# Kernel tuning notes

Measured on AMD Instinct MI355X. Metric: run time of the kernel, lower is better.

The kernel has to match this reference:

```python
import jax, jax.numpy as jnp
import numpy as np

N_NODES = 50000
N_EDGES = 800000
IN_DIM = 128
HID = 128
NUM_CLASSES = 2


def setup_inputs() -> dict:
    key = jax.random.key(0)
    ks = jax.random.split(key, 16)
    inp = {
        "adj_row": jax.random.randint(ks[0], (N_EDGES,), 0, N_NODES),
        "adj_col": jax.random.randint(ks[1], (N_EDGES,), 0, N_NODES),
        "adj_vals": jax.random.uniform(ks[2], (N_EDGES,), dtype=jnp.float32),
        "input_feature": jax.random.normal(ks[3], (N_NODES, IN_DIM), dtype=jnp.float32),
        "graph_indicator": jax.random.randint(ks[4], (N_NODES,), 0, 64),
        # GCN layer params (kaiming-uniform-ish init; zeros bias like the torch module)
        "W1": jax.random.uniform(ks[5], (IN_DIM, HID), jnp.float32, -1, 1) * np.sqrt(6.0 / IN_DIM),
        "b1": jnp.zeros((HID,), jnp.float32),
        "W2": jax.random.uniform(ks[6], (HID, HID), jnp.float32, -1, 1) * np.sqrt(6.0 / HID),
        "b2": jnp.zeros((HID,), jnp.float32),
        "W3": jax.random.uniform(ks[7], (HID, HID), jnp.float32, -1, 1) * np.sqrt(6.0 / HID),
        "b3": jnp.zeros((HID,), jnp.float32),
        # fc params (torch.nn.Linear default init range)
        "fcW1": jax.random.uniform(ks[8], (3 * HID, HID), jnp.float32, -1, 1) / np.sqrt(3 * HID),
        "fcb1": jax.random.uniform(ks[9], (HID,), jnp.float32, -1, 1) / np.sqrt(3 * HID),
        "fcW2": jax.random.uniform(ks[10], (HID, HID // 2), jnp.float32, -1, 1) / np.sqrt(HID),
        "fcb2": jax.random.uniform(ks[11], (HID // 2,), jnp.float32, -1, 1) / np.sqrt(HID),
        "fcW3": jax.random.uniform(ks[12], (HID // 2, NUM_CLASSES), jnp.float32, -1, 1) / np.sqrt(HID // 2),
        "fcb3": jax.random.uniform(ks[13], (NUM_CLASSES,), jnp.float32, -1, 1) / np.sqrt(HID // 2),
    }
    return inp


def _gcn_layer(row, col, vals, x, W, b, n_nodes):
    # support = X @ W  -> dense GEMM
    support = x @ W
    # sparse.mm(A, support): out[i] = sum_{e: row[e]=i} vals[e] * support[col[e]]
    msgs = support[col] * vals[:, None]  # [E, D] gather + scale
    agg = jax.ops.segment_sum(msgs, row, num_segments=n_nodes)
    return agg + b


def reference(adj_row, adj_col, adj_vals, input_feature, graph_indicator,
              W1, b1, W2, b2, W3, b3, fcW1, fcb1, fcW2, fcb2, fcW3, fcb3):
    n = input_feature.shape[0]
    g1 = jax.nn.relu(_gcn_layer(adj_row, adj_col, adj_vals, input_feature, W1, b1, n))
    g2 = jax.nn.relu(_gcn_layer(adj_row, adj_col, adj_vals, g1, W2, b2, n))
    g3 = jax.nn.relu(_gcn_layer(adj_row, adj_col, adj_vals, g2, W3, b3, n))
    feat = jnp.concatenate([g1, g2, g3], axis=1)  # [N, 3*HID]
    h = jax.nn.relu(feat @ fcW1 + fcb1)
    h = jax.nn.relu(h @ fcW2 + fcb2)
    logits = h @ fcW3 + fcb3
    return logits
```

## Files before the change

### kernel.cpp

```cpp
#include <hip/hip_runtime.h>
#include <hip/hip_bf16.h>

#define N_NODES 50000
#define N_EDGES 800000
#define NBK 391
#define BCAP 2560
#define PADSLACK 896

static inline int cdiv(int a, int b) { return (a + b - 1) / b; }

typedef __attribute__((ext_vector_type(8))) short short8;
typedef __attribute__((ext_vector_type(4))) float f32x4;

__device__ __forceinline__ float b2f(unsigned short u) {
    union { unsigned int i; float f; } c;
    c.i = ((unsigned int)u) << 16;
    return c.f;
}
__device__ __forceinline__ unsigned short f2bb(float f) {
    __hip_bfloat16 h = __float2bfloat16(f);
    return *(unsigned short*)&h;
}

__device__ __forceinline__ void pack_one(const float* __restrict__ W,
                                         __hip_bfloat16* __restrict__ out,
                                         int K, int N, int t) {
    int lane = t & 63;
    int kc = (t >> 6) % (K / 32);
    int nt = (t >> 6) / (K / 32);
    int kbase = kc * 32 + (lane >> 4) * 8;
    int col = nt * 16 + (lane & 15);
    __hip_bfloat16* dst = out + (size_t)t * 8;
#pragma unroll
    for (int j = 0; j < 8; ++j)
        dst[j] = __float2bfloat16(W[(size_t)(kbase + j) * N + col]);
}

__global__ __launch_bounds__(256)
void stage1_kernel(const int* __restrict__ row, const int* __restrict__ col,
                   const float* __restrict__ vals, int* __restrict__ bcursor,
                   int2* __restrict__ tmp, int E,
                   const float* __restrict__ x, __hip_bfloat16* __restrict__ support,
                   int M,
                   const float* __restrict__ W1, const float* __restrict__ W2,
                   const float* __restrict__ W3, const float* __restrict__ fcW1,
                   const float* __restrict__ fcW2,
                   __hip_bfloat16* __restrict__ pW2, __hip_bfloat16* __restrict__ pW3,
                   __hip_bfloat16* __restrict__ pfcW1, __hip_bfloat16* __restrict__ pfcW2) {
    __shared__ unsigned short As[64][136];
    __shared__ int hist[NBK];
    __shared__ int base[NBK];
    const int b = blockIdx.x;
    const int tid = threadIdx.x;

    if (b < 196) {
        const int CH = 4096;
        int e0 = b * CH;
        for (int i = tid; i < NBK; i += 256) hist[i] = 0;
        __syncthreads();
        for (int i = tid; i < CH; i += 256) {
            int e = e0 + i;
            if (e < E) atomicAdd(&hist[row[e] >> 7], 1);
        }
        __syncthreads();
        for (int i = tid; i < NBK; i += 256) {
            int c = hist[i];
            base[i] = (c > 0) ? (i * BCAP + atomicAdd(&bcursor[i], c)) : 0;
            hist[i] = 0;
        }
        __syncthreads();
        for (int i = tid; i < CH; i += 256) {
            int e = e0 + i;
            if (e < E) {
                int r = row[e];
                int bk = r >> 7;
                int rk = atomicAdd(&hist[bk], 1);
                tmp[base[bk] + rk] = make_int2(((r & 127) << 16) | col[e],
                                               __float_as_int(vals[e]));
            }
        }
        return;
    }

    if (b < 978) {
        const int wave = tid >> 6;
        const int lane = tid & 63;
        const int ln15 = lane & 15;
        const int quad = lane >> 4;
        const int m0 = (b - 196) * 64;

        short8 bfr[4][2];
#pragma unroll
        for (int kc = 0; kc < 4; ++kc)
#pragma unroll
            for (int h = 0; h < 2; ++h)
#pragma unroll
                for (int j = 0; j < 8; ++j)
                    bfr[kc][h][j] = (short)f2bb(
                        W1[(size_t)(kc * 32 + quad * 8 + j) * 128 + (wave * 2 + h) * 16 + ln15]);

#pragma unroll
        for (int i = 0; i < 4; ++i) {
            int idx = tid + i * 256;
            int r = idx >> 4;
            int c8 = (idx & 15) * 8;
            uint4 pk = {0, 0, 0, 0};
            if (m0 + r < M) {
                const float* src = &x[(size_t)(m0 + r) * 128 + c8];
                float4 a = *(const float4*)src;
                float4 bq = *(const float4*)(src + 4);
                pk.x = f2bb(a.x) | ((unsigned int)f2bb(a.y) << 16);
                pk.y = f2bb(a.z) | ((unsigned int)f2bb(a.w) << 16);
                pk.z = f2bb(bq.x) | ((unsigned int)f2bb(bq.y) << 16);
                pk.w = f2bb(bq.z) | ((unsigned int)f2bb(bq.w) << 16);
            }
            *(uint4*)&As[r][c8] = pk;
        }
        __syncthreads();

        f32x4 acc[4][2];
#pragma unroll
        for (int s = 0; s < 4; ++s)
#pragma unroll
            for (int h = 0; h < 2; ++h) acc[s][h] = (f32x4){0.f, 0.f, 0.f, 0.f};
#pragma unroll
        for (int kc = 0; kc < 4; ++kc) {
            short8 af[4];
#pragma unroll
            for (int s = 0; s < 4; ++s)
                af[s] = *(const short8*)&As[s * 16 + ln15][kc * 32 + quad * 8];
#pragma unroll
            for (int s = 0; s < 4; ++s)
#pragma unroll
                for (int h = 0; h < 2; ++h)
                    acc[s][h] = __builtin_amdgcn_mfma_f32_16x16x32_bf16(
                        af[s], bfr[kc][h], acc[s][h], 0, 0, 0);
        }
#pragma unroll
        for (int s = 0; s < 4; ++s)
#pragma unroll
            for (int h = 0; h < 2; ++h) {
                int cl = (wave * 2 + h) * 16 + ln15;
#pragma unroll
                for (int r = 0; r < 4; ++r) {
                    int rw = m0 + s * 16 + quad * 4 + r;
                    if (rw < M)
                        support[(size_t)rw * 128 + cl] = __float2bfloat16(acc[s][h][r]);
                }
            }
        return;
    }

    int pb = b - 978;
    if (pb < 8)       pack_one(W2,  pW2,  128, 128, pb * 256 + tid);
    else if (pb < 16) pack_one(W3,  pW3,  128, 128, (pb - 8) * 256 + tid);
    else if (pb < 40) pack_one(fcW1, pfcW1, 384, 128, (pb - 16) * 256 + tid);
    else              pack_one(fcW2, pfcW2, 128, 64, (pb - 40) * 256 + tid);
}

__global__ __launch_bounds__(256)
void binB_kernel(const int2* __restrict__ tmp, const int* __restrict__ bcursor,
                 int2* __restrict__ rowrange, int2* __restrict__ epack, int N) {
    int b = blockIdx.x;
    int r0 = b << 7;
    int nr = N - r0; if (nr > 128) nr = 128;
    __shared__ int cnt[128];
    __shared__ int cur[128];
    __shared__ int rpos[128];
    __shared__ int red[256];
    int t = threadIdx.x;
    int partial = 0;
    for (int i = t; i < b; i += 256) partial += bcursor[i];
    red[t] = partial;
    if (t < 128) cnt[t] = 0;
    __syncthreads();
    for (int off = 128; off > 0; off >>= 1) {
        if (t < off) red[t] += red[t + off];
        __syncthreads();
    }
    int slab = b * BCAP;
    int send = slab + bcursor[b];
    for (int i = slab + t; i < send; i += 256)
        atomicAdd(&cnt[tmp[i].x >> 16], 1);
    __syncthreads();
    int rcnt = (t < 128) ? cnt[t] : 0;
    int pc = (rcnt + 7) & ~7;
    if (t < 128) cur[t] = pc;
    __syncthreads();
    for (int off = 1; off < 128; off <<= 1) {
        int u = (t >= off && t < 128) ? cur[t - off] : 0;
        __syncthreads();
        if (t < 128) cur[t] += u;
        __syncthreads();
    }
    int obase = red[0] + b * PADSLACK;
    if (t < 128) {
        int pos = obase + cur[t] - pc;
        rpos[t] = pos;
        cur[t] = pos;
        if (t < nr) rowrange[r0 + t] = make_int2(pos, pos + pc);
    }
    __syncthreads();
    for (int i = slab + t; i < send; i += 256) {
        int2 v = tmp[i];
        int rl = v.x >> 16;
        int c = v.x & 0xffff;
        int pos = atomicAdd(&cur[rl], 1);
        epack[pos] = make_int2(c, v.y);
    }
    if (t < 128) {
        int rc = rcnt;
        int pos = rpos[t];
#pragma unroll 1
        for (int i = pos + rc; i < pos + pc; ++i)
            epack[i] = make_int2(0, 0);
    }
}

__device__ __forceinline__ void accum8(float* acc, long long e, uint4 u) {
    float f = __int_as_float((int)(e >> 32));
    acc[0] += f * b2f((unsigned short)(u.x & 0xffff));
    acc[1] += f * b2f((unsigned short)(u.x >> 16));
    acc[2] += f * b2f((unsigned short)(u.y & 0xffff));
    acc[3] += f * b2f((unsigned short)(u.y >> 16));
    acc[4] += f * b2f((unsigned short)(u.z & 0xffff));
    acc[5] += f * b2f((unsigned short)(u.z >> 16));
    acc[6] += f * b2f((unsigned short)(u.w & 0xffff));
    acc[7] += f * b2f((unsigned short)(u.w >> 16));
}

__device__ __forceinline__ void agg_node(const long long* __restrict__ ep,
                                         const __hip_bfloat16* __restrict__ support,
                                         int p, int end, int g, int j, float* acc) {
#pragma unroll
    for (int k = 0; k < 8; ++k) acc[k] = 0.f;
    long long e0 = 0, e1 = 0;
    uint4 u0 = {0, 0, 0, 0}, u1 = {0, 0, 0, 0};
    bool have = false;
    if (p < end) {
        e0 = ep[p + g];
        e1 = ep[p + 4 + g];
        u0 = *(const uint4*)&support[(size_t)(unsigned int)(e0 & 0xffffffffu) * 128 + j * 8];
        u1 = *(const uint4*)&support[(size_t)(unsigned int)(e1 & 0xffffffffu) * 128 + j * 8];
        p += 8;
        have = true;
    }
    while (p < end) {
        long long f0 = ep[p + g];
        long long f1 = ep[p + 4 + g];
        uint4 w0 = *(const uint4*)&support[(size_t)(unsigned int)(f0 & 0xffffffffu) * 128 + j * 8];
        uint4 w1 = *(const uint4*)&support[(size_t)(unsigned int)(f1 & 0xffffffffu) * 128 + j * 8];
        accum8(acc, e0, u0);
        accum8(acc, e1, u1);
        e0 = f0; u0 = w0; e1 = f1; u1 = w1;
        p += 8;
    }
    if (have) {
        accum8(acc, e0, u0);
        accum8(acc, e1, u1);
    }
#pragma unroll
    for (int k = 0; k < 8; ++k) {
        acc[k] += __shfl_xor(acc[k], 16);
        acc[k] += __shfl_xor(acc[k], 32);
    }
}

__device__ __forceinline__ uint4 pack_row8(const float* acc, float4 b0, float4 b1) {
    unsigned int q0 = (unsigned int)f2bb(fmaxf(acc[0] + b0.x, 0.f))
                    | ((unsigned int)f2bb(fmaxf(acc[1] + b0.y, 0.f)) << 16);
    unsigned int q1 = (unsigned int)f2bb(fmaxf(acc[2] + b0.z, 0.f))
                    | ((unsigned int)f2bb(fmaxf(acc[3] + b0.w, 0.f)) << 16);
    unsigned int q2 = (unsigned int)f2bb(fmaxf(acc[4] + b1.x, 0.f))
                    | ((unsigned int)f2bb(fmaxf(acc[5] + b1.y, 0.f)) << 16);
    unsigned int q3 = (unsigned int)f2bb(fmaxf(acc[6] + b1.z, 0.f))
                    | ((unsigned int)f2bb(fmaxf(acc[7] + b1.w, 0.f)) << 16);
    return (uint4){q0, q1, q2, q3};
}

__global__ __launch_bounds__(256, 8)
void spmm_gemm_kernel(const int2* __restrict__ rowrange,
                      const int2* __restrict__ epack,
                      const __hip_bfloat16* __restrict__ support,
                      const float* __restrict__ bias,
                      __hip_bfloat16* __restrict__ gout,
                      const __hip_bfloat16* __restrict__ pW,
                      __hip_bfloat16* __restrict__ Cout,
                      int N) {
    __shared__ unsigned short As[16][136];
    const int tid = threadIdx.x;
    const int wv = tid >> 6;
    const int l = tid & 63;
    const int g = l >> 4;
    const int j = l & 15;
    const int m0 = blockIdx.x * 16;
    const long long* ep = (const long long*)epack;
    float4 b0 = *(const float4*)&bias[j * 8];
    float4 b1 = *(const float4*)&bias[j * 8 + 4];

    for (int i = 0; i < 4; ++i) {
        int node = m0 + wv * 4 + i;
        if (node < N) {
            int2 rr = rowrange[node];
            float acc[8];
            agg_node(ep, support, rr.x, rr.y, g, j, acc);
            if (g == 0) {
                uint4 st = pack_row8(acc, b0, b1);
                *(uint4*)&As[wv * 4 + i][j * 8] = st;
                *(uint4*)&gout[(size_t)node * 384 + j * 8] = st;
            }
        } else if (g == 0) {
            *(uint4*)&As[wv * 4 + i][j * 8] = (uint4){0, 0, 0, 0};
        }
    }
    __syncthreads();

    const int ln15 = l & 15;
    const int quad = l >> 4;
    f32x4 acc2[2];
    acc2[0] = (f32x4){0.f, 0.f, 0.f, 0.f};
    acc2[1] = (f32x4){0.f, 0.f, 0.f, 0.f};
#pragma unroll
    for (int kc = 0; kc < 4; ++kc) {
        short8 af = *(const short8*)&As[ln15][kc * 32 + quad * 8];
#pragma unroll
        for (int h = 0; h < 2; ++h) {
            int nt = wv * 2 + h;
            short8 bf = *(const short8*)&pW[((size_t)(nt * 4 + kc) * 64 + l) * 8];
            acc2[h] = __builtin_amdgcn_mfma_f32_16x16x32_bf16(af, bf, acc2[h], 0, 0, 0);
        }
    }
#pragma unroll
    for (int h = 0; h < 2; ++h) {
        int cl = (wv * 2 + h) * 16 + ln15;
#pragma unroll
        for (int r = 0; r < 4; ++r) {
            int rw = m0 + quad * 4 + r;
            if (rw < N)
                Cout[(size_t)rw * 128 + cl] = __float2bfloat16(acc2[h][r]);
        }
    }
}

__global__ __launch_bounds__(256, 8)
void spmm_fc_kernel(const int2* __restrict__ rowrange,
                    const int2* __restrict__ epack,
                    const __hip_bfloat16* __restrict__ support,
                    const float* __restrict__ bias,
                    const __hip_bfloat16* __restrict__ featb,
                    const __hip_bfloat16* __restrict__ pfcW1,
                    const float* __restrict__ fcb1,
                    const __hip_bfloat16* __restrict__ pfcW2,
                    const float* __restrict__ fcb2,
                    const float* __restrict__ fcW3, const float* __restrict__ fcb3,
                    float* __restrict__ out, int N) {
    __shared__ unsigned short As[16][136];
    __shared__ float w3s[128];
    __shared__ float b3s[2];
    const int tid = threadIdx.x;
    const int wv = tid >> 6;
    const int l = tid & 63;
    const int g = l >> 4;
    const int j = l & 15;
    const int m0 = blockIdx.x * 16;
    const long long* ep = (const long long*)epack;
    if (tid < 128) w3s[tid] = fcW3[tid];
    if (tid < 2) b3s[tid] = fcb3[tid];
    float4 b0 = *(const float4*)&bias[j * 8];
    float4 b1 = *(const float4*)&bias[j * 8 + 4];

    for (int i = 0; i < 4; ++i) {
        int node = m0 + wv * 4 + i;
        if (node < N) {
            int2 rr = rowrange[node];
            float acc[8];
            agg_node(ep, support, rr.x, rr.y, g, j, acc);
            if (g == 0)
                *(uint4*)&As[wv * 4 + i][j * 8] = pack_row8(acc, b0, b1);
        } else if (g == 0) {
            *(uint4*)&As[wv * 4 + i][j * 8] = (uint4){0, 0, 0, 0};
        }
    }
    __syncthreads();

    const int ln15 = l & 15;
    const int quad = l >> 4;
    f32x4 acc[2];
    acc[0] = (f32x4){0.f, 0.f, 0.f, 0.f};
    acc[1] = (f32x4){0.f, 0.f, 0.f, 0.f};
#pragma unroll
    for (int step = 0; step < 3; ++step) {
        const int kb = (step == 0) ? 2 : (step - 1);
        if (step != 0) {
            __syncthreads();
            int r = tid >> 4;
            int c8 = (tid & 15) * 8;
            *(uint4*)&As[r][c8] =
                *(const uint4*)&featb[(size_t)(m0 + r) * 384 + kb * 128 + c8];
            __syncthreads();
        }
#pragma unroll
        for (int kc = 0; kc < 4; ++kc) {
            short8 af = *(const short8*)&As[ln15][kc * 32 + quad * 8];
            int kcg = kb * 4 + kc;
#pragma unroll
            for (int h = 0; h < 2; ++h) {
                int nt = wv * 2 + h;
                short8 bf = *(const short8*)&pfcW1[((size_t)(nt * 12 + kcg) * 64 + l) * 8];
                acc[h] = __builtin_amdgcn_mfma_f32_16x16x32_bf16(af, bf, acc[h], 0, 0, 0);
            }
        }
    }
    __syncthreads();
#pragma unroll
    for (int h = 0; h < 2; ++h) {
        int col = (wv * 2 + h) * 16 + ln15;
        float bv = fcb1[col];
#pragma unroll
        for (int r = 0; r < 4; ++r)
            As[quad * 4 + r][col] = f2bb(fmaxf(acc[h][r] + bv, 0.f));
    }
    __syncthreads();

    f32x4 acc2 = (f32x4){0.f, 0.f, 0.f, 0.f};
#pragma unroll
    for (int kc = 0; kc < 4; ++kc) {
        short8 af = *(const short8*)&As[ln15][kc * 32 + quad * 8];
        short8 bfw = *(const short8*)&pfcW2[((size_t)(wv * 4 + kc) * 64 + l) * 8];
        acc2 = __builtin_amdgcn_mfma_f32_16x16x32_bf16(af, bfw, acc2, 0, 0, 0);
    }
    __syncthreads();
    {
        int col2 = wv * 16 + ln15;
        float bv = fcb2[col2];
#pragma unroll
        for (int r = 0; r < 4; ++r)
            As[quad * 4 + r][col2] = f2bb(fmaxf(acc2[r] + bv, 0.f));
    }
    __syncthreads();

    if (tid < 32) {
        int row = tid >> 1, cls = tid & 1;
        int grow = m0 + row;
        if (grow < N) {
            float a = b3s[cls];
#pragma unroll
            for (int k = 0; k < 64; ++k)
                a += b2f(As[row][k]) * w3s[k * 2 + cls];
            out[(size_t)grow * 2 + cls] = a;
        }
    }
}

extern "C" void kernel_launch(void* const* d_in, const int* in_sizes, int n_in,
                              void* d_out, int out_size, void* d_ws, size_t ws_size,
                              hipStream_t stream) {
    const int*   adj_row  = (const int*)d_in[0];
    const int*   adj_col  = (const int*)d_in[1];
    const float* adj_vals = (const float*)d_in[2];
    const float* x        = (const float*)d_in[3];
    const float* W1   = (const float*)d_in[5];
    const float* b1   = (const float*)d_in[6];
    const float* W2   = (const float*)d_in[7];
    const float* b2   = (const float*)d_in[8];
    const float* W3   = (const float*)d_in[9];
    const float* b3   = (const float*)d_in[10];
    const float* fcW1 = (const float*)d_in[11];
    const float* fcb1 = (const float*)d_in[12];
    const float* fcW2 = (const float*)d_in[13];
    const float* fcb2 = (const float*)d_in[14];
    const float* fcW3 = (const float*)d_in[15];
    const float* fcb3 = (const float*)d_in[16];
    float* out = (float*)d_out;

    const int N = N_NODES, E = N_EDGES;
    const int Mpad = 50048;
    const int EPAD = E + NBK * PADSLACK + 64;

    char* p = (char*)d_ws;
    auto alloc = [&](size_t bytes) {
        char* q = p;
        p += (bytes + 255) & ~(size_t)255;
        return q;
    };
    __hip_bfloat16* featb    = (__hip_bfloat16*)alloc((size_t)Mpad * 384 * 2);
    __hip_bfloat16* supportb = (__hip_bfloat16*)alloc((size_t)Mpad * 128 * 2);
    __hip_bfloat16* supportc = (__hip_bfloat16*)alloc((size_t)Mpad * 128 * 2);
    __hip_bfloat16* pW2   = (__hip_bfloat16*)alloc(16384 * 2);
    __hip_bfloat16* pW3   = (__hip_bfloat16*)alloc(16384 * 2);
    __hip_bfloat16* pfcW1 = (__hip_bfloat16*)alloc(49152 * 2);
    __hip_bfloat16* pfcW2 = (__hip_bfloat16*)alloc(8192 * 2);
    int2*  rowrange  = (int2*)alloc((size_t)(N + 1) * 8);
    int*   bcursor   = (int*)alloc((size_t)NBK * 4);
    int2*  epack     = (int2*)alloc((size_t)EPAD * 8);
    int2*  tmp       = (int2*)alloc((size_t)NBK * BCAP * 8);

    hipMemsetAsync(bcursor, 0, (size_t)NBK * 4, stream);
    stage1_kernel<<<1022, 256, 0, stream>>>(adj_row, adj_col, adj_vals, bcursor, tmp, E,
                                            x, supportb, N,
                                            W1, W2, W3, fcW1, fcW2,
                                            pW2, pW3, pfcW1, pfcW2);
    binB_kernel<<<NBK, 256, 0, stream>>>(tmp, bcursor, rowrange, epack, N);

    const int fgrid = cdiv(N, 16);

    spmm_gemm_kernel<<<fgrid, 256, 0, stream>>>(rowrange, epack, supportb, b1,
                                                featb + 0, pW2, supportc, N);
    spmm_gemm_kernel<<<fgrid, 256, 0, stream>>>(rowrange, epack, supportc, b2,
                                                featb + 128, pW3, supportb, N);
    spmm_fc_kernel<<<fgrid, 256, 0, stream>>>(rowrange, epack, supportb, b3,
                                              featb, pfcW1, fcb1, pfcW2, fcb2,
                                              fcW3, fcb3, out, N);
}
```

Before: 252.3 us.

## Bin edges by 16-row blocks and fuse per-row sort into first SpMM

Edge binning now uses 16-row buckets matching the SpMM tile, and the separate binB kernel is removed. The first SpMM+GEMM kernel counts and scatters its own bucket into per-row padded ranges before aggregating, dropping one kernel launch and the global prefix scan. The trade-off is a larger shared histogram in stage1 (3125 bins), fixed per-bucket capacities of 448 edges that could overflow on skewed graphs, and a serial 16-row scan inside each block.

```diff
diff --git a/kernel.cpp b/kernel.cpp
--- a/kernel.cpp
+++ b/kernel.cpp
@@ -3,9 +3,9 @@
 
 #define N_NODES 50000
 #define N_EDGES 800000
-#define NBK 391
-#define BCAP 2560
-#define PADSLACK 896
+#define NB16 3125
+#define BCAP16 448
+#define REG16 560
 
 static inline int cdiv(int a, int b) { return (a + b - 1) / b; }
 
@@ -47,36 +47,37 @@
                    const float* __restrict__ fcW2,
                    __hip_bfloat16* __restrict__ pW2, __hip_bfloat16* __restrict__ pW3,
                    __hip_bfloat16* __restrict__ pfcW1, __hip_bfloat16* __restrict__ pfcW2) {
-    __shared__ unsigned short As[64][136];
-    __shared__ int hist[NBK];
-    __shared__ int base[NBK];
+    __shared__ union {
+        unsigned short As[64][136];
+        struct { int hist[NB16]; int base[NB16]; } bin;
+    } sh;
     const int b = blockIdx.x;
     const int tid = threadIdx.x;
 
     if (b < 196) {
         const int CH = 4096;
         int e0 = b * CH;
-        for (int i = tid; i < NBK; i += 256) hist[i] = 0;
+        for (int i = tid; i < NB16; i += 256) sh.bin.hist[i] = 0;
         __syncthreads();
         for (int i = tid; i < CH; i += 256) {
             int e = e0 + i;
-            if (e < E) atomicAdd(&hist[row[e] >> 7], 1);
+            if (e < E) atomicAdd(&sh.bin.hist[row[e] >> 4], 1);
         }
         __syncthreads();
-        for (int i = tid; i < NBK; i += 256) {
-            int c = hist[i];
-            base[i] = (c > 0) ? (i * BCAP + atomicAdd(&bcursor[i], c)) : 0;
-            hist[i] = 0;
+        for (int i = tid; i < NB16; i += 256) {
+            int c = sh.bin.hist[i];
+            sh.bin.base[i] = (c > 0) ? (i * BCAP16 + atomicAdd(&bcursor[i], c)) : 0;
+            sh.bin.hist[i] = 0;
         }
         __syncthreads();
         for (int i = tid; i < CH; i += 256) {
             int e = e0 + i;
             if (e < E) {
                 int r = row[e];
-                int bk = r >> 7;
-                int rk = atomicAdd(&hist[bk], 1);
-                tmp[base[bk] + rk] = make_int2(((r & 127) << 16) | col[e],
-                                               __float_as_int(vals[e]));
+                int bk = r >> 4;
+                int rk = atomicAdd(&sh.bin.hist[bk], 1);
+                tmp[sh.bin.base[bk] + rk] = make_int2(((r & 15) << 16) | col[e],
+                                                      __float_as_int(vals[e]));
             }
         }
         return;
@@ -114,7 +115,7 @@
                 pk.z = f2bb(bq.x) | ((unsigned int)f2bb(bq.y) << 16);
                 pk.w = f2bb(bq.z) | ((unsigned int)f2bb(bq.w) << 16);
             }
-            *(uint4*)&As[r][c8] = pk;
+            *(uint4*)&sh.As[r][c8] = pk;
         }
         __syncthreads();
 
@@ -128,7 +129,7 @@
             short8 af[4];
 #pragma unroll
             for (int s = 0; s < 4; ++s)
-                af[s] = *(const short8*)&As[s * 16 + ln15][kc * 32 + quad * 8];
+                af[s] = *(const short8*)&sh.As[s * 16 + ln15][kc * 32 + quad * 8];
 #pragma unroll
             for (int s = 0; s < 4; ++s)
 #pragma unroll
@@ -156,65 +157,6 @@
     else if (pb < 16) pack_one(W3,  pW3,  128, 128, (pb - 8) * 256 + tid);
     else if (pb < 40) pack_one(fcW1, pfcW1, 384, 128, (pb - 16) * 256 + tid);
     else              pack_one(fcW2, pfcW2, 128, 64, (pb - 40) * 256 + tid);
-}
-
-__global__ __launch_bounds__(256)
-void binB_kernel(const int2* __restrict__ tmp, const int* __restrict__ bcursor,
-                 int2* __restrict__ rowrange, int2* __restrict__ epack, int N) {
-    int b = blockIdx.x;
-    int r0 = b << 7;
-    int nr = N - r0; if (nr > 128) nr = 128;
-    __shared__ int cnt[128];
-    __shared__ int cur[128];
-    __shared__ int rpos[128];
-    __shared__ int red[256];
-    int t = threadIdx.x;
-    int partial = 0;
-    for (int i = t; i < b; i += 256) partial += bcursor[i];
-    red[t] = partial;
-    if (t < 128) cnt[t] = 0;
-    __syncthreads();
-    for (int off = 128; off > 0; off >>= 1) {
-        if (t < off) red[t] += red[t + off];
-        __syncthreads();
-    }
-    int slab = b * BCAP;
-    int send = slab + bcursor[b];
-    for (int i = slab + t; i < send; i += 256)
-        atomicAdd(&cnt[tmp[i].x >> 16], 1);
-    __syncthreads();
-    int rcnt = (t < 128) ? cnt[t] : 0;
-    int pc = (rcnt + 7) & ~7;
-    if (t < 128) cur[t] = pc;
-    __syncthreads();
-    for (int off = 1; off < 128; off <<= 1) {
-        int u = (t >= off && t < 128) ? cur[t - off] : 0;
-        __syncthreads();
-        if (t < 128) cur[t] += u;
-        __syncthreads();
-    }
-    int obase = red[0] + b * PADSLACK;
-    if (t < 128) {
-        int pos = obase + cur[t] - pc;
-        rpos[t] = pos;
-        cur[t] = pos;
-        if (t < nr) rowrange[r0 + t] = make_int2(pos, pos + pc);
-    }
-    __syncthreads();
-    for (int i = slab + t; i < send; i += 256) {
-        int2 v = tmp[i];
-        int rl = v.x >> 16;
-        int c = v.x & 0xffff;
-        int pos = atomicAdd(&cur[rl], 1);
-        epack[pos] = make_int2(c, v.y);
-    }
-    if (t < 128) {
-        int rc = rcnt;
-        int pos = rpos[t];
-#pragma unroll 1
-        for (int i = pos + rc; i < pos + pc; ++i)
-            epack[i] = make_int2(0, 0);
-    }
 }
 
 __device__ __forceinline__ void accum8(float* acc, long long e, uint4 u) {
@@ -276,6 +218,109 @@
     unsigned int q3 = (unsigned int)f2bb(fmaxf(acc[6] + b1.z, 0.f))
                     | ((unsigned int)f2bb(fmaxf(acc[7] + b1.w, 0.f)) << 16);
     return (uint4){q0, q1, q2, q3};
+}
+
+__global__ __launch_bounds__(256, 8)
+void spmm_sort_gemm_kernel(const int2* __restrict__ tmp,
+                           const int* __restrict__ bcursor,
+                           int2* __restrict__ rowrange, int2* __restrict__ epack,
+                           const __hip_bfloat16* __restrict__ support,
+                           const float* __restrict__ bias,
+                           __hip_bfloat16* __restrict__ gout,
+                           const __hip_bfloat16* __restrict__ pW,
+                           __hip_bfloat16* __restrict__ Cout,
+                           int N) {
+    __shared__ unsigned short As[16][136];
+    __shared__ int cnt[16];
+    __shared__ int cur[16];
+    __shared__ int rpos[16];
+    const int b = blockIdx.x;
+    const int tid = threadIdx.x;
+    const int wv = tid >> 6;
+    const int l = tid & 63;
+    const int g = l >> 4;
+    const int j = l & 15;
+    const int m0 = b * 16;
+    const int r0 = m0;
+
+    if (tid < 16) cnt[tid] = 0;
+    __syncthreads();
+    int slab = b * BCAP16;
+    int send = slab + bcursor[b];
+    for (int i = slab + tid; i < send; i += 256)
+        atomicAdd(&cnt[tmp[i].x >> 16], 1);
+    __syncthreads();
+    if (tid == 0) {
+        int pos = b * REG16;
+#pragma unroll 1
+        for (int k = 0; k < 16; ++k) {
+            int rc = cnt[k];
+            int pc = (rc + 7) & ~7;
+            rpos[k] = pos;
+            cur[k] = pos;
+            rowrange[r0 + k] = make_int2(pos, pos + pc);
+            pos += pc;
+        }
+    }
+    __syncthreads();
+    for (int i = slab + tid; i < send; i += 256) {
+        int2 v = tmp[i];
+        int rl = v.x >> 16;
+        int pos = atomicAdd(&cur[rl], 1);
+        epack[pos] = make_int2(v.x & 0xffff, v.y);
+    }
+    if (tid < 16) {
+        int rc = cnt[tid];
+        int pc = (rc + 7) & ~7;
+        int pos = rpos[tid];
+#pragma unroll 1
+        for (int i = pos + rc; i < pos + pc; ++i)
+            epack[i] = make_int2(0, 0);
+    }
+    __syncthreads();
+
+    const long long* ep = (const long long*)epack;
+    float4 b0 = *(const float4*)&bias[j * 8];
+    float4 b1 = *(const float4*)&bias[j * 8 + 4];
+    for (int i = 0; i < 4; ++i) {
+        int i0 = wv * 4 + i;
+        int ps = rpos[i0];
+        int pe = ps + ((cnt[i0] + 7) & ~7);
+        float acc[8];
+        agg_node(ep, support, ps, pe, g, j, acc);
+        if (g == 0) {
+            uint4 st = pack_row8(acc, b0, b1);
+            *(uint4*)&As[i0][j * 8] = st;
+            *(uint4*)&gout[(size_t)(m0 + i0) * 384 + j * 8] = st;
+        }
+    }
+    __syncthreads();
+
+    const int ln15 = l & 15;
+    const int quad = l >> 4;
+    f32x4 acc2[2];
+    acc2[0] = (f32x4){0.f, 0.f, 0.f, 0.f};
+    acc2[1] = (f32x4){0.f, 0.f, 0.f, 0.f};
+#pragma unroll
+    for (int kc = 0; kc < 4; ++kc) {
+        short8 af = *(const short8*)&As[ln15][kc * 32 + quad * 8];
+#pragma unroll
+        for (int h = 0; h < 2; ++h) {
+            int nt = wv * 2 + h;
+            short8 bf = *(const short8*)&pW[((size_t)(nt * 4 + kc) * 64 + l) * 8];
+            acc2[h] = __builtin_amdgcn_mfma_f32_16x16x32_bf16(af, bf, acc2[h], 0, 0, 0);
+        }
+    }
+#pragma unroll
+    for (int h = 0; h < 2; ++h) {
+        int cl = (wv * 2 + h) * 16 + ln15;
+#pragma unroll
+        for (int r = 0; r < 4; ++r) {
+            int rw = m0 + quad * 4 + r;
+            if (rw < N)
+                Cout[(size_t)rw * 128 + cl] = __float2bfloat16(acc2[h][r]);
+        }
+    }
 }
 
 __global__ __launch_bounds__(256, 8)
@@ -475,7 +520,6 @@
 
     const int N = N_NODES, E = N_EDGES;
     const int Mpad = 50048;
-    const int EPAD = E + NBK * PADSLACK + 64;
 
     char* p = (char*)d_ws;
     auto alloc = [&](size_t bytes) {
@@ -491,21 +535,21 @@
     __hip_bfloat16* pfcW1 = (__hip_bfloat16*)alloc(49152 * 2);
     __hip_bfloat16* pfcW2 = (__hip_bfloat16*)alloc(8192 * 2);
     int2*  rowrange  = (int2*)alloc((size_t)(N + 1) * 8);
-    int*   bcursor   = (int*)alloc((size_t)NBK * 4);
-    int2*  epack     = (int2*)alloc((size_t)EPAD * 8);
-    int2*  tmp       = (int2*)alloc((size_t)NBK * BCAP * 8);
-
-    hipMemsetAsync(bcursor, 0, (size_t)NBK * 4, stream);
+    int*   bcursor   = (int*)alloc((size_t)NB16 * 4);
+    int2*  epack     = (int2*)alloc((size_t)NB16 * REG16 * 8 + 256);
+    int2*  tmp       = (int2*)alloc((size_t)NB16 * BCAP16 * 8);
+
+    hipMemsetAsync(bcursor, 0, (size_t)NB16 * 4, stream);
     stage1_kernel<<<1022, 256, 0, stream>>>(adj_row, adj_col, adj_vals, bcursor, tmp, E,
                                             x, supportb, N,
                                             W1, W2, W3, fcW1, fcW2,
                                             pW2, pW3, pfcW1, pfcW2);
-    binB_kernel<<<NBK, 256, 0, stream>>>(tmp, bcursor, rowrange, epack, N);
-
-    const int fgrid = cdiv(N, 16);
-
-    spmm_gemm_kernel<<<fgrid, 256, 0, stream>>>(rowrange, epack, supportb, b1,
-                                                featb + 0, pW2, supportc, N);
+
+    const int fgrid = NB16;
+
+    spmm_sort_gemm_kernel<<<fgrid, 256, 0, stream>>>(tmp, bcursor, rowrange, epack,
+                                                     supportb, b1, featb + 0,
+                                                     pW2, supportc, N);
     spmm_gemm_kernel<<<fgrid, 256, 0, stream>>>(rowrange, epack, supportc, b2,
                                                 featb + 128, pW3, supportb, N);
     spmm_fc_kernel<<<fgrid, 256, 0, stream>>>(rowrange, epack, supportb, b3,
```

Measured after the change: 257.3 us. No clear change (+2.0%).
